# Kernel tuning notes

Measured on AMD Instinct MI355X. Metric: run time of the kernel, lower is better.

## Reference

```python
import jax, jax.numpy as jnp
import numpy as np

N = 100000        # number of nodes
D_IN = 256        # input feature dim
D_OUT = 128       # output feature dim
NNZ_X = 3200000   # features_nonzero
NNZ_A = 3200000   # adjacency nnz (avg degree 32)
DROPOUT = 0.1


def setup_inputs() -> dict:
    key = jax.random.key(0)
    ks = jax.random.split(key, 7)
    x_rows = jax.random.randint(ks[0], (NNZ_X,), 0, N, dtype=jnp.int32)
    x_cols = jax.random.randint(ks[1], (NNZ_X,), 0, D_IN, dtype=jnp.int32)
    x_vals = jax.random.normal(ks[2], (NNZ_X,), dtype=jnp.float32)
    adj_rows = jax.random.randint(ks[3], (NNZ_A,), 0, N, dtype=jnp.int32)
    adj_cols = jax.random.randint(ks[4], (NNZ_A,), 0, N, dtype=jnp.int32)
    adj_vals = jax.random.uniform(ks[5], (NNZ_A,), dtype=jnp.float32)  # normalized-adj-like positive weights
    W = jax.random.normal(ks[6], (D_IN, D_OUT), dtype=jnp.float32) * 0.05  # 'random_normal' init
    return {"x_rows": x_rows, "x_cols": x_cols, "x_vals": x_vals,
            "adj_rows": adj_rows, "adj_cols": adj_cols, "adj_vals": adj_vals,
            "W": W}


def reference(x_rows, x_cols, x_vals, adj_rows, adj_cols, adj_vals, W):
    keep_prob = 1.0 - DROPOUT
    # tf: dropout_mask = floor(keep_prob + uniform) -> Bernoulli(keep_prob) in {0,1}
    mask = jnp.floor(keep_prob + jax.random.uniform(jax.random.key(42), x_vals.shape, dtype=x_vals.dtype))
    xv = x_vals * mask * (1.0 / keep_prob)  # sparse dropout: retain + rescale
    # SpMM 1: x @ W  -> h [N, D_OUT]; gather W rows by column index, scatter-add by row index
    h = jax.ops.segment_sum(xv[:, None] * W[x_cols], x_rows, num_segments=N)
    # SpMM 2: adj @ h -> out [N, D_OUT]
    out = jax.ops.segment_sum(adj_vals[:, None] * h[adj_cols], adj_rows, num_segments=N)
    return jax.nn.relu(out)
```

## Files before the change

kernel.cpp:

```cpp
#include <hip/hip_runtime.h>
#include <hip/hip_fp16.h>
#include <hip/hip_bf16.h>
#include <stdint.h>

constexpr int kN    = 100000;
constexpr int kDOut = 128;
constexpr int kDIn  = 256;
constexpr int kNNZ  = 3200000;
constexpr float kInvKeep = (float)(1.0 / 0.9);
constexpr int kCopies  = 8;
constexpr int kBktRows = kN / 8;

typedef __attribute__((ext_vector_type(8))) short short8v;
typedef __attribute__((ext_vector_type(4))) float f32x4;

__device__ __forceinline__ uint32_t rotl32(uint32_t v, int r) {
  return (v << r) | (v >> (32 - r));
}
__device__ __forceinline__ void threefry2x32(uint32_t k0, uint32_t k1,
                                             uint32_t x0, uint32_t x1,
                                             uint32_t& o0, uint32_t& o1) {
  const uint32_t ks0 = k0, ks1 = k1, ks2 = k0 ^ k1 ^ 0x1BD11BDAu;
  x0 += ks0; x1 += ks1;
#define TF_RND(r) { x0 += x1; x1 = rotl32(x1, (r)); x1 ^= x0; }
  TF_RND(13) TF_RND(15) TF_RND(26) TF_RND(6)
  x0 += ks1; x1 += ks2 + 1u;
  TF_RND(17) TF_RND(29) TF_RND(16) TF_RND(24)
  x0 += ks2; x1 += ks0 + 2u;
  TF_RND(13) TF_RND(15) TF_RND(26) TF_RND(6)
  x0 += ks0; x1 += ks1 + 3u;
  TF_RND(17) TF_RND(29) TF_RND(16) TF_RND(24)
  x0 += ks1; x1 += ks2 + 4u;
  TF_RND(13) TF_RND(15) TF_RND(26) TF_RND(6)
  x0 += ks2; x1 += ks0 + 5u;
#undef TF_RND
  o0 = x0; o1 = x1;
}
__device__ __forceinline__ float keep_mask(uint32_t i) {
  uint32_t o0, o1;
  threefry2x32(0u, 42u, 0u, i, o0, o1);
  uint32_t bits = o0 ^ o1;
  float u = __uint_as_float((bits >> 9) | 0x3f800000u) - 1.0f;
  return floorf(0.9f + u);
}

__device__ __forceinline__ uint32_t f32_to_bf16(float f) {
  uint32_t u = __float_as_uint(f);
  u += 0x7fffu + ((u >> 16) & 1u);
  return u >> 16;
}
__device__ __forceinline__ float bf16lo_to_f32(uint32_t packed) {
  return __uint_as_float(packed << 16);
}
__device__ __forceinline__ float bf16hi_to_f32(uint32_t packed) {
  return __uint_as_float(packed & 0xffff0000u);
}

__global__ void wpack_frag_kernel(const float* __restrict__ W,
                                  uint32_t* __restrict__ Wt) {
  int i = blockIdx.x * blockDim.x + threadIdx.x;
  if (i >= kDIn * kDOut / 2) return;
  int jj   = i & 3;
  int lane = (i >> 2) & 63;
  int ks   = (i >> 8) & 7;
  int nt   = i >> 11;
  int n = nt * 16 + (lane & 15);
  int k = ks * 32 + ((lane >> 4) * 8) + 2 * jj;
  uint32_t lo = f32_to_bf16(W[(size_t)k * kDOut + n]);
  uint32_t hi = f32_to_bf16(W[(size_t)(k + 1) * kDOut + n]);
  Wt[i] = lo | (hi << 16);
}

__global__ void scatteradd_kernel(const int* __restrict__ rows,
                                  const int* __restrict__ cols,
                                  const float* __restrict__ vals,
                                  __hip_bfloat162* __restrict__ Xd2, int nnz) {
  int e = blockIdx.x * blockDim.x + threadIdx.x;
  if (e >= nnz) return;
  if (keep_mask((uint32_t)e) == 0.0f) return;
  int r = rows[e], c = cols[e];
  float v = vals[e] * kInvKeep;
  uint32_t pk = f32_to_bf16(v) << ((c & 1) ? 16 : 0);
  __hip_bfloat162 val = *reinterpret_cast<__hip_bfloat162*>(&pk);
  unsafeAtomicAdd(&Xd2[((size_t)r * kDIn + c) >> 1], val);
}

__global__ void __launch_bounds__(256) gemm_mfma_kernel(
    const uint16_t* __restrict__ Xd, const uint32_t* __restrict__ Wt,
    uint16_t* __restrict__ hb) {
  const int tid = threadIdx.x;
  const int gw = blockIdx.x * 4 + (tid >> 6);
  if (gw >= kN / 16) return;
  const int lane = tid & 63;
  const int row16 = gw * 16;
  const uint16_t* xrow =
      Xd + (size_t)(row16 + (lane & 15)) * kDIn + ((lane >> 4) * 8);

  f32x4 acc[8];
  #pragma unroll
  for (int nt = 0; nt < 8; ++nt) acc[nt] = f32x4{0.f, 0.f, 0.f, 0.f};

  #pragma unroll
  for (int ks = 0; ks < 8; ++ks) {
    short8v a = *(const short8v*)(xrow + ks * 32);
    const uint32_t* bbase = Wt + ks * 256 + lane * 4;
    #pragma unroll
    for (int nt = 0; nt < 8; ++nt) {
      short8v b = *(const short8v*)(bbase + nt * 2048);
      acc[nt] = __builtin_amdgcn_mfma_f32_16x16x32_bf16(a, b, acc[nt], 0, 0, 0);
    }
  }

  const int r0 = row16 + (lane >> 4) * 4;
  const int c0 = lane & 15;
  #pragma unroll
  for (int nt = 0; nt < 8; ++nt) {
    #pragma unroll
    for (int rg = 0; rg < 4; ++rg) {
      hb[(size_t)(r0 + rg) * kDOut + nt * 16 + c0] =
          (uint16_t)f32_to_bf16(acc[nt][rg]);
    }
  }
}

__global__ void hist8_kernel(const int* __restrict__ rows, int* __restrict__ cnt8,
                             int nnz) {
  int e = blockIdx.x * blockDim.x + threadIdx.x;
  if (e >= nnz) return;
  int k = blockIdx.x & (kCopies - 1);
  atomicAdd(&cnt8[k * kN + rows[e]], 1);
}

constexpr int kScanChunk = 2048;
constexpr int kScanBlk   = (kN + kScanChunk - 1) / kScanChunk;

__global__ void scan1_kernel(const int* __restrict__ cnt8, int* __restrict__ rowptr,
                             int* __restrict__ partials, int n) {
  __shared__ int sd[256];
  int b = blockIdx.x, t = threadIdx.x;
  int base = b * kScanChunk + t * 8;
  int v[8]; int s = 0;
  #pragma unroll
  for (int k = 0; k < 8; ++k) {
    int idx = base + k;
    int c = 0;
    if (idx < n) {
      #pragma unroll
      for (int j = 0; j < kCopies; ++j) c += cnt8[j * kN + idx];
    }
    v[k] = c; s += c;
  }
  sd[t] = s; __syncthreads();
  #pragma unroll
  for (int off = 1; off < 256; off <<= 1) {
    int x = (t >= off) ? sd[t - off] : 0;
    __syncthreads();
    sd[t] += x;
    __syncthreads();
  }
  if (t == 255) partials[b] = sd[255];
  int run = (t == 0) ? 0 : sd[t - 1];
  #pragma unroll
  for (int k = 0; k < 8; ++k) { int idx = base + k; if (idx < n) rowptr[idx] = run; run += v[k]; }
}

__global__ void scan2_kernel(int* __restrict__ partials, int* __restrict__ rowptr,
                             int nblk, int n) {
  __shared__ int sd[64];
  int t = threadIdx.x;
  sd[t] = (t < nblk) ? partials[t] : 0;
  __syncthreads();
  #pragma unroll
  for (int off = 1; off < 64; off <<= 1) {
    int x = (t >= off) ? sd[t - off] : 0;
    __syncthreads();
    sd[t] += x;
    __syncthreads();
  }
  if (t < nblk) partials[t] = (t == 0) ? 0 : sd[t - 1];
  if (t == 63) rowptr[n] = sd[63];
}

__global__ void scan3_kernel(int* __restrict__ rowptr, int* __restrict__ cur,
                             int* __restrict__ bcur,
                             const int* __restrict__ partials, int n) {
  int i = blockIdx.x * blockDim.x + threadIdx.x;
  if (i < n) {
    int v = rowptr[i] + partials[i / kScanChunk];
    rowptr[i] = v;
    cur[i] = v;
    if ((i % kBktRows) == 0) bcur[i / kBktRows] = v;
  }
}

__global__ void __launch_bounds__(256) passA_kernel(
    const int* __restrict__ rows, const int* __restrict__ cols,
    const float* __restrict__ vals, int* __restrict__ bcur,
    uint2* __restrict__ P, int nnz) {
  __shared__ int lcnt[8];
  __shared__ int gbase[8];
  const int tid = threadIdx.x;
  const int base = blockIdx.x * 4096;
  if (tid < 8) lcnt[tid] = 0;
  __syncthreads();
  int c0 = 0, c1 = 0, c2 = 0, c3 = 0, c4 = 0, c5 = 0, c6 = 0, c7 = 0;
  for (int i = 0; i < 16; ++i) {
    int e = base + i * 256 + tid;
    if (e < nnz) {
      int b = rows[e] / kBktRows;
      if (b < 4) {
        if (b < 2) { if (b == 0) c0++; else c1++; }
        else       { if (b == 2) c2++; else c3++; }
      } else {
        if (b < 6) { if (b == 4) c4++; else c5++; }
        else       { if (b == 6) c6++; else c7++; }
      }
    }
  }
  if (c0) atomicAdd(&lcnt[0], c0);
  if (c1) atomicAdd(&lcnt[1], c1);
  if (c2) atomicAdd(&lcnt[2], c2);
  if (c3) atomicAdd(&lcnt[3], c3);
  if (c4) atomicAdd(&lcnt[4], c4);
  if (c5) atomicAdd(&lcnt[5], c5);
  if (c6) atomicAdd(&lcnt[6], c6);
  if (c7) atomicAdd(&lcnt[7], c7);
  __syncthreads();
  if (tid < 8) {
    gbase[tid] = atomicAdd(&bcur[tid], lcnt[tid]);
    lcnt[tid] = 0;
  }
  __syncthreads();
  for (int i = 0; i < 16; ++i) {
    int e = base + i * 256 + tid;
    if (e >= nnz) continue;
    int r = rows[e];
    int b = r / kBktRows;
    int lpos = atomicAdd(&lcnt[b], 1);
    uint2 rec;
    rec.x = ((uint32_t)(r % kBktRows) << 17) | (uint32_t)cols[e];
    rec.y = __float_as_uint(vals[e]);
    P[gbase[b] + lpos] = rec;
  }
}

__global__ void passB_kernel(const int* __restrict__ rowptr,
                             const uint2* __restrict__ P,
                             int* __restrict__ cur,
                             uint32_t* __restrict__ spack) {
  const int k = blockIdx.x & 7;
  const int slot = blockIdx.x >> 3;
  const int nslots = gridDim.x >> 3;
  const int lorow = k * kBktRows;
  const int s = rowptr[lorow];
  const int t = rowptr[lorow + kBktRows];
  for (int idx = s + slot * 256 + threadIdx.x; idx < t; idx += nslots * 256) {
    uint2 rec = P[idx];
    int r = lorow + (int)(rec.x >> 17);
    int pos = atomicAdd(&cur[r], 1);
    float v = __uint_as_float(rec.y);
    uint32_t h = (uint32_t)__half_as_ushort(__float2half_rn(v)) & 0x7FFFu;
    spack[pos] = ((rec.x & 0x1FFFFu) << 15) | h;
  }
}

template<bool RELU>
__global__ void spmm_csr_kernel(const int* __restrict__ rowptr,
                                const uint32_t* __restrict__ spack,
                                const uint16_t* __restrict__ B,
                                float* __restrict__ outv, int nrows) {
  int tid = threadIdx.x;
  int row = blockIdx.x * 4 + (tid >> 6);
  int lane = tid & 63;
  if (row >= nrows) return;
  int e = rowptr[row], e_end = rowptr[row + 1];
  float a0 = 0.0f, a1 = 0.0f;
  const int doff = lane * 2;
  auto dec = [](uint32_t p) -> float {
    return __half2float(__ushort_as_half((unsigned short)(p & 0x7FFFu)));
  };
  for (; e + 7 < e_end; e += 8) {
    uint32_t p0 = spack[e],     p1 = spack[e + 1];
    uint32_t p2 = spack[e + 2], p3 = spack[e + 3];
    uint32_t p4 = spack[e + 4], p5 = spack[e + 5];
    uint32_t p6 = spack[e + 6], p7 = spack[e + 7];
    uint32_t g0 = *(const uint32_t*)(B + (size_t)(p0 >> 15) * kDOut + doff);
    uint32_t g1 = *(const uint32_t*)(B + (size_t)(p1 >> 15) * kDOut + doff);
    uint32_t g2 = *(const uint32_t*)(B + (size_t)(p2 >> 15) * kDOut + doff);
    uint32_t g3 = *(const uint32_t*)(B + (size_t)(p3 >> 15) * kDOut + doff);
    uint32_t g4 = *(const uint32_t*)(B + (size_t)(p4 >> 15) * kDOut + doff);
    uint32_t g5 = *(const uint32_t*)(B + (size_t)(p5 >> 15) * kDOut + doff);
    uint32_t g6 = *(const uint32_t*)(B + (size_t)(p6 >> 15) * kDOut + doff);
    uint32_t g7 = *(const uint32_t*)(B + (size_t)(p7 >> 15) * kDOut + doff);
    float v0 = dec(p0), v1 = dec(p1), v2 = dec(p2), v3 = dec(p3);
    float v4 = dec(p4), v5 = dec(p5), v6 = dec(p6), v7 = dec(p7);
    a0 += v0 * bf16lo_to_f32(g0); a1 += v0 * bf16hi_to_f32(g0);
    a0 += v1 * bf16lo_to_f32(g1); a1 += v1 * bf16hi_to_f32(g1);
    a0 += v2 * bf16lo_to_f32(g2); a1 += v2 * bf16hi_to_f32(g2);
    a0 += v3 * bf16lo_to_f32(g3); a1 += v3 * bf16hi_to_f32(g3);
    a0 += v4 * bf16lo_to_f32(g4); a1 += v4 * bf16hi_to_f32(g4);
    a0 += v5 * bf16lo_to_f32(g5); a1 += v5 * bf16hi_to_f32(g5);
    a0 += v6 * bf16lo_to_f32(g6); a1 += v6 * bf16hi_to_f32(g6);
    a0 += v7 * bf16lo_to_f32(g7); a1 += v7 * bf16hi_to_f32(g7);
  }
  for (; e < e_end; ++e) {
    uint32_t p0 = spack[e];
    float v0 = dec(p0);
    uint32_t g0 = *(const uint32_t*)(B + (size_t)(p0 >> 15) * kDOut + doff);
    a0 += v0 * bf16lo_to_f32(g0);
    a1 += v0 * bf16hi_to_f32(g0);
  }
  if (RELU) { a0 = fmaxf(a0, 0.0f); a1 = fmaxf(a1, 0.0f); }
  float2 o; o.x = a0; o.y = a1;
  ((float2*)outv)[(size_t)row * (kDOut / 2) + lane] = o;
}

extern "C" void kernel_launch(void* const* d_in, const int* in_sizes, int n_in,
                              void* d_out, int out_size, void* d_ws, size_t ws_size,
                              hipStream_t stream) {
  const int*   x_rows   = (const int*)d_in[0];
  const int*   x_cols   = (const int*)d_in[1];
  const float* x_vals   = (const float*)d_in[2];
  const int*   adj_rows = (const int*)d_in[3];
  const int*   adj_cols = (const int*)d_in[4];
  const float* adj_vals = (const float*)d_in[5];
  const float* W        = (const float*)d_in[6];
  float* out = (float*)d_out;

  size_t off = 0;
  auto take = [&](size_t bytes) -> char* {
    char* p = (char*)d_ws + off;
    off += (bytes + 255) & ~(size_t)255;
    return p;
  };
  uint16_t* hb     = (uint16_t*)take((size_t)kN * kDOut * 2);
  uint32_t* Wt     = (uint32_t*)take((size_t)kDIn * kDOut / 2 * 4);
  int*      rowptr = (int*)take((size_t)(kN + 1) * 4);
  int*      cnt8   = (int*)take((size_t)kCopies * kN * 4);
  int*      cur    = (int*)take((size_t)kN * 4);
  int*      bcur   = (int*)take(8 * 4);
  int*      partials = (int*)take(64 * 4);
  uint32_t* spack  = (uint32_t*)take((size_t)kNNZ * 4);
  uint16_t* Xd     = (uint16_t*)take((size_t)kN * kDIn * 2);
  const size_t needed = off;
  if (ws_size < needed) return;
  uint2*    P = (uint2*)Xd;

  const int edgeBlocks = (kNNZ + 255) / 256;
  const int spmmBlocks = (kN + 3) / 4;
  const int gemmBlocks = (kN / 16 + 3) / 4;
  const int passABlocks = (kNNZ + 4095) / 4096;
  const int passBBlocks = 8 * 1664;

  wpack_frag_kernel<<<(kDIn * kDOut / 2 + 255) / 256, 256, 0, stream>>>(W, Wt);

  hipMemsetAsync(Xd, 0, (size_t)kN * kDIn * 2, stream);
  scatteradd_kernel<<<edgeBlocks, 256, 0, stream>>>(
      x_rows, x_cols, x_vals, (__hip_bfloat162*)Xd, kNNZ);
  gemm_mfma_kernel<<<gemmBlocks, 256, 0, stream>>>(Xd, Wt, hb);

  hipMemsetAsync(cnt8, 0, (size_t)kCopies * kN * 4, stream);
  hist8_kernel<<<edgeBlocks, 256, 0, stream>>>(adj_rows, cnt8, kNNZ);
  scan1_kernel<<<kScanBlk, 256, 0, stream>>>(cnt8, rowptr, partials, kN);
  scan2_kernel<<<1, 64, 0, stream>>>(partials, rowptr, kScanBlk, kN);
  scan3_kernel<<<(kN + 255) / 256, 256, 0, stream>>>(rowptr, cur, bcur, partials, kN);
  passA_kernel<<<passABlocks, 256, 0, stream>>>(
      adj_rows, adj_cols, adj_vals, bcur, P, kNNZ);
  passB_kernel<<<passBBlocks, 256, 0, stream>>>(rowptr, P, cur, spack);
  spmm_csr_kernel<true><<<spmmBlocks, 256, 0, stream>>>(
      rowptr, spack, hb, out, kN);
}
```

Before: 609.1 us.

## Fuse independent kernels horizontally: scatter-add with histogram, GEMM with bucket pass

Merges the feature scatter-add and adjacency histogram into one launch using block-index ranges, and merges the MFMA GEMM with the bucketing pass A into another. The goal is to run independent work side by side so that two atomic-bound or memory-bound phases overlap and fewer launches sit on the critical path. P no longer aliases Xd and gets its own workspace buffer, which adds a 25.6 MB allocation. The GEMM and passA blocks share one kernel with different resource needs, so occupancy may be limited by the heavier branch.

```diff
diff --git a/kernel.cpp b/kernel.cpp
--- a/kernel.cpp
+++ b/kernel.cpp
@@ -10,6 +10,10 @@
 constexpr float kInvKeep = (float)(1.0 / 0.9);
 constexpr int kCopies  = 8;
 constexpr int kBktRows = kN / 8;
+
+constexpr int kEdgeBlocks = (kNNZ + 255) / 256;
+constexpr int kGemmBlocks = (kN / 16 + 3) / 4;
+constexpr int kPassABlocks = (kNNZ + 4095) / 4096;
 
 typedef __attribute__((ext_vector_type(8))) short short8v;
 typedef __attribute__((ext_vector_type(4))) float f32x4;
@@ -71,64 +75,27 @@
   Wt[i] = lo | (hi << 16);
 }
 
-__global__ void scatteradd_kernel(const int* __restrict__ rows,
-                                  const int* __restrict__ cols,
-                                  const float* __restrict__ vals,
-                                  __hip_bfloat162* __restrict__ Xd2, int nnz) {
-  int e = blockIdx.x * blockDim.x + threadIdx.x;
-  if (e >= nnz) return;
-  if (keep_mask((uint32_t)e) == 0.0f) return;
-  int r = rows[e], c = cols[e];
-  float v = vals[e] * kInvKeep;
-  uint32_t pk = f32_to_bf16(v) << ((c & 1) ? 16 : 0);
-  __hip_bfloat162 val = *reinterpret_cast<__hip_bfloat162*>(&pk);
-  unsafeAtomicAdd(&Xd2[((size_t)r * kDIn + c) >> 1], val);
-}
-
-__global__ void __launch_bounds__(256) gemm_mfma_kernel(
-    const uint16_t* __restrict__ Xd, const uint32_t* __restrict__ Wt,
-    uint16_t* __restrict__ hb) {
-  const int tid = threadIdx.x;
-  const int gw = blockIdx.x * 4 + (tid >> 6);
-  if (gw >= kN / 16) return;
-  const int lane = tid & 63;
-  const int row16 = gw * 16;
-  const uint16_t* xrow =
-      Xd + (size_t)(row16 + (lane & 15)) * kDIn + ((lane >> 4) * 8);
-
-  f32x4 acc[8];
-  #pragma unroll
-  for (int nt = 0; nt < 8; ++nt) acc[nt] = f32x4{0.f, 0.f, 0.f, 0.f};
-
-  #pragma unroll
-  for (int ks = 0; ks < 8; ++ks) {
-    short8v a = *(const short8v*)(xrow + ks * 32);
-    const uint32_t* bbase = Wt + ks * 256 + lane * 4;
-    #pragma unroll
-    for (int nt = 0; nt < 8; ++nt) {
-      short8v b = *(const short8v*)(bbase + nt * 2048);
-      acc[nt] = __builtin_amdgcn_mfma_f32_16x16x32_bf16(a, b, acc[nt], 0, 0, 0);
-    }
-  }
-
-  const int r0 = row16 + (lane >> 4) * 4;
-  const int c0 = lane & 15;
-  #pragma unroll
-  for (int nt = 0; nt < 8; ++nt) {
-    #pragma unroll
-    for (int rg = 0; rg < 4; ++rg) {
-      hb[(size_t)(r0 + rg) * kDOut + nt * 16 + c0] =
-          (uint16_t)f32_to_bf16(acc[nt][rg]);
-    }
-  }
-}
-
-__global__ void hist8_kernel(const int* __restrict__ rows, int* __restrict__ cnt8,
-                             int nnz) {
-  int e = blockIdx.x * blockDim.x + threadIdx.x;
-  if (e >= nnz) return;
-  int k = blockIdx.x & (kCopies - 1);
-  atomicAdd(&cnt8[k * kN + rows[e]], 1);
+__global__ void __launch_bounds__(256) fused_sa_hist_kernel(
+    const int* __restrict__ x_rows, const int* __restrict__ x_cols,
+    const float* __restrict__ x_vals, __hip_bfloat162* __restrict__ Xd2,
+    const int* __restrict__ adj_rows, int* __restrict__ cnt8) {
+  const int bid = blockIdx.x;
+  if (bid < kEdgeBlocks) {
+    int e = bid * 256 + threadIdx.x;
+    if (e >= kNNZ) return;
+    if (keep_mask((uint32_t)e) == 0.0f) return;
+    int r = x_rows[e], c = x_cols[e];
+    float v = x_vals[e] * kInvKeep;
+    uint32_t pk = f32_to_bf16(v) << ((c & 1) ? 16 : 0);
+    __hip_bfloat162 val = *reinterpret_cast<__hip_bfloat162*>(&pk);
+    unsafeAtomicAdd(&Xd2[((size_t)r * kDIn + c) >> 1], val);
+  } else {
+    int b = bid - kEdgeBlocks;
+    int e = b * 256 + threadIdx.x;
+    if (e >= kNNZ) return;
+    int k = b & (kCopies - 1);
+    atomicAdd(&cnt8[k * kN + adj_rows[e]], 1);
+  }
 }
 
 constexpr int kScanChunk = 2048;
@@ -193,54 +160,92 @@
   }
 }
 
-__global__ void __launch_bounds__(256) passA_kernel(
+__global__ void __launch_bounds__(256) fused_gemm_passA_kernel(
+    const uint16_t* __restrict__ Xd, const uint32_t* __restrict__ Wt,
+    uint16_t* __restrict__ hb,
     const int* __restrict__ rows, const int* __restrict__ cols,
     const float* __restrict__ vals, int* __restrict__ bcur,
-    uint2* __restrict__ P, int nnz) {
+    uint2* __restrict__ P) {
   __shared__ int lcnt[8];
   __shared__ int gbase[8];
   const int tid = threadIdx.x;
-  const int base = blockIdx.x * 4096;
-  if (tid < 8) lcnt[tid] = 0;
-  __syncthreads();
-  int c0 = 0, c1 = 0, c2 = 0, c3 = 0, c4 = 0, c5 = 0, c6 = 0, c7 = 0;
-  for (int i = 0; i < 16; ++i) {
-    int e = base + i * 256 + tid;
-    if (e < nnz) {
-      int b = rows[e] / kBktRows;
-      if (b < 4) {
-        if (b < 2) { if (b == 0) c0++; else c1++; }
-        else       { if (b == 2) c2++; else c3++; }
-      } else {
-        if (b < 6) { if (b == 4) c4++; else c5++; }
-        else       { if (b == 6) c6++; else c7++; }
+
+  if (blockIdx.x < kGemmBlocks) {
+    const int gw = blockIdx.x * 4 + (tid >> 6);
+    if (gw >= kN / 16) return;
+    const int lane = tid & 63;
+    const int row16 = gw * 16;
+    const uint16_t* xrow =
+        Xd + (size_t)(row16 + (lane & 15)) * kDIn + ((lane >> 4) * 8);
+
+    f32x4 acc[8];
+    #pragma unroll
+    for (int nt = 0; nt < 8; ++nt) acc[nt] = f32x4{0.f, 0.f, 0.f, 0.f};
+
+    #pragma unroll
+    for (int ks = 0; ks < 8; ++ks) {
+      short8v a = *(const short8v*)(xrow + ks * 32);
+      const uint32_t* bbase = Wt + ks * 256 + lane * 4;
+      #pragma unroll
+      for (int nt = 0; nt < 8; ++nt) {
+        short8v b = *(const short8v*)(bbase + nt * 2048);
+        acc[nt] = __builtin_amdgcn_mfma_f32_16x16x32_bf16(a, b, acc[nt], 0, 0, 0);
       }
     }
-  }
-  if (c0) atomicAdd(&lcnt[0], c0);
-  if (c1) atomicAdd(&lcnt[1], c1);
-  if (c2) atomicAdd(&lcnt[2], c2);
-  if (c3) atomicAdd(&lcnt[3], c3);
-  if (c4) atomicAdd(&lcnt[4], c4);
-  if (c5) atomicAdd(&lcnt[5], c5);
-  if (c6) atomicAdd(&lcnt[6], c6);
-  if (c7) atomicAdd(&lcnt[7], c7);
-  __syncthreads();
-  if (tid < 8) {
-    gbase[tid] = atomicAdd(&bcur[tid], lcnt[tid]);
-    lcnt[tid] = 0;
-  }
-  __syncthreads();
-  for (int i = 0; i < 16; ++i) {
-    int e = base + i * 256 + tid;
-    if (e >= nnz) continue;
-    int r = rows[e];
-    int b = r / kBktRows;
-    int lpos = atomicAdd(&lcnt[b], 1);
-    uint2 rec;
-    rec.x = ((uint32_t)(r % kBktRows) << 17) | (uint32_t)cols[e];
-    rec.y = __float_as_uint(vals[e]);
-    P[gbase[b] + lpos] = rec;
+
+    const int r0 = row16 + (lane >> 4) * 4;
+    const int c0 = lane & 15;
+    #pragma unroll
+    for (int nt = 0; nt < 8; ++nt) {
+      #pragma unroll
+      for (int rg = 0; rg < 4; ++rg) {
+        hb[(size_t)(r0 + rg) * kDOut + nt * 16 + c0] =
+            (uint16_t)f32_to_bf16(acc[nt][rg]);
+      }
+    }
+  } else {
+    const int base = (blockIdx.x - kGemmBlocks) * 4096;
+    if (tid < 8) lcnt[tid] = 0;
+    __syncthreads();
+    int c0 = 0, c1 = 0, c2 = 0, c3 = 0, c4 = 0, c5 = 0, c6 = 0, c7 = 0;
+    for (int i = 0; i < 16; ++i) {
+      int e = base + i * 256 + tid;
+      if (e < kNNZ) {
+        int b = rows[e] / kBktRows;
+        if (b < 4) {
+          if (b < 2) { if (b == 0) c0++; else c1++; }
+          else       { if (b == 2) c2++; else c3++; }
+        } else {
+          if (b < 6) { if (b == 4) c4++; else c5++; }
+          else       { if (b == 6) c6++; else c7++; }
+        }
+      }
+    }
+    if (c0) atomicAdd(&lcnt[0], c0);
+    if (c1) atomicAdd(&lcnt[1], c1);
+    if (c2) atomicAdd(&lcnt[2], c2);
+    if (c3) atomicAdd(&lcnt[3], c3);
+    if (c4) atomicAdd(&lcnt[4], c4);
+    if (c5) atomicAdd(&lcnt[5], c5);
+    if (c6) atomicAdd(&lcnt[6], c6);
+    if (c7) atomicAdd(&lcnt[7], c7);
+    __syncthreads();
+    if (tid < 8) {
+      gbase[tid] = atomicAdd(&bcur[tid], lcnt[tid]);
+      lcnt[tid] = 0;
+    }
+    __syncthreads();
+    for (int i = 0; i < 16; ++i) {
+      int e = base + i * 256 + tid;
+      if (e >= kNNZ) continue;
+      int r = rows[e];
+      int b = r / kBktRows;
+      int lpos = atomicAdd(&lcnt[b], 1);
+      uint2 rec;
+      rec.x = ((uint32_t)(r % kBktRows) << 17) | (uint32_t)cols[e];
+      rec.y = __float_as_uint(vals[e]);
+      P[gbase[b] + lpos] = rec;
+    }
   }
 }
 
@@ -342,30 +347,27 @@
   int*      partials = (int*)take(64 * 4);
   uint32_t* spack  = (uint32_t*)take((size_t)kNNZ * 4);
   uint16_t* Xd     = (uint16_t*)take((size_t)kN * kDIn * 2);
+  uint2*    P      = (uint2*)take((size_t)kNNZ * 8);
   const size_t needed = off;
   if (ws_size < needed) return;
-  uint2*    P = (uint2*)Xd;
-
-  const int edgeBlocks = (kNNZ + 255) / 256;
+
   const int spmmBlocks = (kN + 3) / 4;
-  const int gemmBlocks = (kN / 16 + 3) / 4;
-  const int passABlocks = (kNNZ + 4095) / 4096;
   const int passBBlocks = 8 * 1664;
 
+  hipMemsetAsync(Xd, 0, (size_t)kN * kDIn * 2, stream);
+  hipMemsetAsync(cnt8, 0, (size_t)kCopies * kN * 4, stream);
   wpack_frag_kernel<<<(kDIn * kDOut / 2 + 255) / 256, 256, 0, stream>>>(W, Wt);
 
-  hipMemsetAsync(Xd, 0, (size_t)kN * kDIn * 2, stream);
-  scatteradd_kernel<<<edgeBlocks, 256, 0, stream>>>(
-      x_rows, x_cols, x_vals, (__hip_bfloat162*)Xd, kNNZ);
-  gemm_mfma_kernel<<<gemmBlocks, 256, 0, stream>>>(Xd, Wt, hb);
-
-  hipMemsetAsync(cnt8, 0, (size_t)kCopies * kN * 4, stream);
-  hist8_kernel<<<edgeBlocks, 256, 0, stream>>>(adj_rows, cnt8, kNNZ);
+  fused_sa_hist_kernel<<<2 * kEdgeBlocks, 256, 0, stream>>>(
+      x_rows, x_cols, x_vals, (__hip_bfloat162*)Xd, adj_rows, cnt8);
+
   scan1_kernel<<<kScanBlk, 256, 0, stream>>>(cnt8, rowptr, partials, kN);
   scan2_kernel<<<1, 64, 0, stream>>>(partials, rowptr, kScanBlk, kN);
   scan3_kernel<<<(kN + 255) / 256, 256, 0, stream>>>(rowptr, cur, bcur, partials, kN);
-  passA_kernel<<<passABlocks, 256, 0, stream>>>(
-      adj_rows, adj_cols, adj_vals, bcur, P, kNNZ);
+
+  fused_gemm_passA_kernel<<<kGemmBlocks + kPassABlocks, 256, 0, stream>>>(
+      Xd, Wt, hb, adj_rows, adj_cols, adj_vals, bcur, P);
+
   passB_kernel<<<passBBlocks, 256, 0, stream>>>(rowptr, P, cur, spack);
   spmm_csr_kernel<true><<<spmmBlocks, 256, 0, stream>>>(
       rowptr, spack, hb, out, kN);
```

Result: no change. 613.3 us (+0.7%).

## Bucket feature nonzeros by row range before scatter-adding into dense X

Applied to the files above, without the earlier changes.

Replaces the direct per-edge bf16 atomic scatter into the dense feature matrix with a two-pass approach. The first pass applies dropout and partitions surviving nonzeros into 8 row buckets. The second pass scatters each bucket using blocks grouped by bucket (blockIdx & 7), so the atomics for one row range are issued together and may stay resident in a single XCD's L2. This costs an extra read and write of a packed record array and a separate workspace buffer, no longer aliased with Xd, plus two extra small launches.

```diff
diff --git a/kernel.cpp b/kernel.cpp
--- a/kernel.cpp
+++ b/kernel.cpp
@@ -10,6 +10,7 @@
 constexpr float kInvKeep = (float)(1.0 / 0.9);
 constexpr int kCopies  = 8;
 constexpr int kBktRows = kN / 8;
+constexpr int kCapX    = kNNZ / 8;
 
 typedef __attribute__((ext_vector_type(8))) short short8v;
 typedef __attribute__((ext_vector_type(4))) float f32x4;
@@ -71,18 +72,80 @@
   Wt[i] = lo | (hi << 16);
 }
 
-__global__ void scatteradd_kernel(const int* __restrict__ rows,
-                                  const int* __restrict__ cols,
-                                  const float* __restrict__ vals,
-                                  __hip_bfloat162* __restrict__ Xd2, int nnz) {
-  int e = blockIdx.x * blockDim.x + threadIdx.x;
-  if (e >= nnz) return;
-  if (keep_mask((uint32_t)e) == 0.0f) return;
-  int r = rows[e], c = cols[e];
-  float v = vals[e] * kInvKeep;
-  uint32_t pk = f32_to_bf16(v) << ((c & 1) ? 16 : 0);
-  __hip_bfloat162 val = *reinterpret_cast<__hip_bfloat162*>(&pk);
-  unsafeAtomicAdd(&Xd2[((size_t)r * kDIn + c) >> 1], val);
+__global__ void seedx_kernel(int* __restrict__ bcurX) {
+  if (threadIdx.x < 8) bcurX[threadIdx.x] = threadIdx.x * kCapX;
+}
+
+__global__ void __launch_bounds__(256) passAx_kernel(
+    const int* __restrict__ rows, const int* __restrict__ cols,
+    const float* __restrict__ vals, int* __restrict__ bcurX,
+    uint2* __restrict__ PX, int nnz) {
+  __shared__ int lcnt[8];
+  __shared__ int gbase[8];
+  const int tid = threadIdx.x;
+  const int base = blockIdx.x * 4096;
+  if (tid < 8) lcnt[tid] = 0;
+  __syncthreads();
+  int c0 = 0, c1 = 0, c2 = 0, c3 = 0, c4 = 0, c5 = 0, c6 = 0, c7 = 0;
+  for (int i = 0; i < 16; ++i) {
+    int e = base + i * 256 + tid;
+    if (e < nnz && keep_mask((uint32_t)e) != 0.0f) {
+      int b = rows[e] / kBktRows;
+      if (b < 4) {
+        if (b < 2) { if (b == 0) c0++; else c1++; }
+        else       { if (b == 2) c2++; else c3++; }
+      } else {
+        if (b < 6) { if (b == 4) c4++; else c5++; }
+        else       { if (b == 6) c6++; else c7++; }
+      }
+    }
+  }
+  if (c0) atomicAdd(&lcnt[0], c0);
+  if (c1) atomicAdd(&lcnt[1], c1);
+  if (c2) atomicAdd(&lcnt[2], c2);
+  if (c3) atomicAdd(&lcnt[3], c3);
+  if (c4) atomicAdd(&lcnt[4], c4);
+  if (c5) atomicAdd(&lcnt[5], c5);
+  if (c6) atomicAdd(&lcnt[6], c6);
+  if (c7) atomicAdd(&lcnt[7], c7);
+  __syncthreads();
+  if (tid < 8) {
+    gbase[tid] = atomicAdd(&bcurX[tid], lcnt[tid]);
+    lcnt[tid] = 0;
+  }
+  __syncthreads();
+  for (int i = 0; i < 16; ++i) {
+    int e = base + i * 256 + tid;
+    if (e >= nnz) continue;
+    if (keep_mask((uint32_t)e) == 0.0f) continue;
+    int r = rows[e];
+    int b = r / kBktRows;
+    int lpos = atomicAdd(&lcnt[b], 1);
+    uint2 rec;
+    rec.x = ((uint32_t)(r % kBktRows) << 8) | (uint32_t)cols[e];
+    rec.y = __float_as_uint(vals[e] * kInvKeep);
+    PX[gbase[b] + lpos] = rec;
+  }
+}
+
+__global__ void sa_local_kernel(const uint2* __restrict__ PX,
+                                const int* __restrict__ bcurX,
+                                __hip_bfloat162* __restrict__ Xd2) {
+  const int k = blockIdx.x & 7;
+  const int slot = blockIdx.x >> 3;
+  const int nslots = gridDim.x >> 3;
+  const int s = k * kCapX;
+  const int t = bcurX[k];
+  const size_t rowbase = (size_t)k * kBktRows;
+  for (int idx = s + slot * 256 + threadIdx.x; idx < t; idx += nslots * 256) {
+    uint2 rec = PX[idx];
+    int rl = (int)(rec.x >> 8);
+    int c  = (int)(rec.x & 255u);
+    float v = __uint_as_float(rec.y);
+    uint32_t pk = f32_to_bf16(v) << ((c & 1) ? 16 : 0);
+    __hip_bfloat162 val = *reinterpret_cast<__hip_bfloat162*>(&pk);
+    unsafeAtomicAdd(&Xd2[((rowbase + rl) * kDIn + c) >> 1], val);
+  }
 }
 
 __global__ void __launch_bounds__(256) gemm_mfma_kernel(
@@ -339,34 +402,38 @@
   int*      cnt8   = (int*)take((size_t)kCopies * kN * 4);
   int*      cur    = (int*)take((size_t)kN * 4);
   int*      bcur   = (int*)take(8 * 4);
+  int*      bcurX  = (int*)take(8 * 4);
   int*      partials = (int*)take(64 * 4);
   uint32_t* spack  = (uint32_t*)take((size_t)kNNZ * 4);
   uint16_t* Xd     = (uint16_t*)take((size_t)kN * kDIn * 2);
+  uint2*    P      = (uint2*)take((size_t)kNNZ * 8);
   const size_t needed = off;
   if (ws_size < needed) return;
-  uint2*    P = (uint2*)Xd;
-
-  const int edgeBlocks = (kNNZ + 255) / 256;
-  const int spmmBlocks = (kN + 3) / 4;
-  const int gemmBlocks = (kN / 16 + 3) / 4;
+
+  const int edgeBlocks  = (kNNZ + 255) / 256;
+  const int spmmBlocks  = (kN + 3) / 4;
+  const int gemmBlocks  = (kN / 16 + 3) / 4;
   const int passABlocks = (kNNZ + 4095) / 4096;
-  const int passBBlocks = 8 * 1664;
-
+  const int pinnedBlocks = 8 * 1664;
+
+  hipMemsetAsync(Xd, 0, (size_t)kN * kDIn * 2, stream);
+  hipMemsetAsync(cnt8, 0, (size_t)kCopies * kN * 4, stream);
   wpack_frag_kernel<<<(kDIn * kDOut / 2 + 255) / 256, 256, 0, stream>>>(W, Wt);
-
-  hipMemsetAsync(Xd, 0, (size_t)kN * kDIn * 2, stream);
-  scatteradd_kernel<<<edgeBlocks, 256, 0, stream>>>(
-      x_rows, x_cols, x_vals, (__hip_bfloat162*)Xd, kNNZ);
+  seedx_kernel<<<1, 64, 0, stream>>>(bcurX);
+
+  passAx_kernel<<<passABlocks, 256, 0, stream>>>(
+      x_rows, x_cols, x_vals, bcurX, P, kNNZ);
+  sa_local_kernel<<<pinnedBlocks, 256, 0, stream>>>(
+      P, bcurX, (__hip_bfloat162*)Xd);
   gemm_mfma_kernel<<<gemmBlocks, 256, 0, stream>>>(Xd, Wt, hb);
 
-  hipMemsetAsync(cnt8, 0, (size_t)kCopies * kN * 4, stream);
   hist8_kernel<<<edgeBlocks, 256, 0, stream>>>(adj_rows, cnt8, kNNZ);
   scan1_kernel<<<kScanBlk, 256, 0, stream>>>(cnt8, rowptr, partials, kN);
   scan2_kernel<<<1, 64, 0, stream>>>(partials, rowptr, kScanBlk, kN);
   scan3_kernel<<<(kN + 255) / 256, 256, 0, stream>>>(rowptr, cur, bcur, partials, kN);
   passA_kernel<<<passABlocks, 256, 0, stream>>>(
       adj_rows, adj_cols, adj_vals, bcur, P, kNNZ);
-  passB_kernel<<<passBBlocks, 256, 0, stream>>>(rowptr, P, cur, spack);
+  passB_kernel<<<pinnedBlocks, 256, 0, stream>>>(rowptr, P, cur, spack);
   spmm_csr_kernel<true><<<spmmBlocks, 256, 0, stream>>>(
       rowptr, spack, hb, out, kN);
 }
```

Result: slower. 673.2 us (+10.5%).
